# Kernel optimization log

Hardware: AMD Instinct MI355X
Metric: run time of the kernel (lower is better)

The kernel has to match this reference:

```python
import jax, jax.numpy as jnp
import numpy as np

H = 100
N = 262144

def setup_inputs() -> dict:
    key = jax.random.key(0)
    ks = jax.random.split(key, 9)
    s = 1.0 / np.sqrt(H)
    return {
        "m": jax.random.normal(ks[0], (1, H), jnp.float32),
        "output_hidden": jax.random.normal(ks[1], (1, 1, H), jnp.float32),
        "fact_embeddings": jax.random.normal(ks[2], (N, H), jnp.float32),
        "W1": jax.random.normal(ks[3], (H, 2 * H), jnp.float32) * s,
        "b1": jax.random.normal(ks[4], (H,), jnp.float32) * s,
        "W2": jax.random.normal(ks[5], (1, H), jnp.float32) * s,
        "b2": jax.random.normal(ks[6], (1,), jnp.float32) * s,
        "W3": jax.random.normal(ks[7], (H, 3 * H), jnp.float32) * s,
        "b3": jax.random.normal(ks[8], (H,), jnp.float32) * s,
    }

def reference(m, output_hidden, fact_embeddings, W1, b1, W2, b2, W3, b3):
    output_context = output_hidden[0]                      # [1, H]
    # z = [|f - oh| ; |f - m|]  -> [N, 2H] (broadcast over N)
    z = jnp.concatenate(
        [jnp.abs(fact_embeddings - output_context),
         jnp.abs(fact_embeddings - m)], axis=1)
    # MLP attention scores, softmax over N facts
    g = jnp.tanh(z @ W1.T + b1) @ W2.T + b2                # [N, 1]
    g = jax.nn.softmax(g.ravel())                          # [N]
    # Weighted-sum pooling of facts
    c = (g[:, None] * fact_embeddings).sum(axis=0, keepdims=True)  # [1, H]
    # Gated memory update
    m_new = jax.nn.relu(jnp.concatenate([m, c, output_context], axis=1) @ W3.T + b3)
    return m_new
```

## Files before the change

kernel.cpp:

```cpp
#include <hip/hip_runtime.h>
#include <hip/hip_bf16.h>
#include <math.h>

#define HDIM 100
#define NFACT 262144
#define FPB   128
#define NBLK_T 2048
#define TPB   4
#define GRID  (NBLK_T / TPB)
#define NTHREADS 512

#define KHALF 112
#define NJT 7
#define NKC 7
#define NBFRAG (NJT * NKC * 64)

#define NCOPY 116
#define NSTRIPE 4

using short8 = __attribute__((ext_vector_type(8))) short;
using f32x4  = __attribute__((ext_vector_type(4))) float;

#define WS_B    0
#define WS_ACC  12544

__device__ __forceinline__ unsigned short f2bf(float x) {
    unsigned u = __builtin_bit_cast(unsigned, x);
    u += 0x7FFFu + ((u >> 16) & 1u);
    return (unsigned short)(u >> 16);
}

__device__ __forceinline__ float tanh_fast(float x) {
    float e = __expf(2.0f * x);
    return 1.0f - 2.0f / (1.0f + e);
}

__global__ __launch_bounds__(256) void k_prep_b(const float* __restrict__ W1,
                                                float* __restrict__ ws) {
    int tg = blockIdx.x * 256 + threadIdx.x;
    if (tg < NSTRIPE * NCOPY) ws[WS_ACC + tg] = 0.f;
    if (tg >= NBFRAG) return;
    int lane = tg & 63;
    int kc = (tg >> 6) % NKC;
    int jt = tg / (NKC * 64);
    int g = lane >> 4, r = lane & 15;
    int j = jt * 16 + r;
    unsigned short v[8];
    #pragma unroll
    for (int e = 0; e < 8; e++) {
        int kglob = kc * 32 + g * 8 + e;
        int half = (kglob >= KHALF) ? 1 : 0;
        int koff = kglob - half * KHALF;
        float x = 0.f;
        if (j < HDIM && koff < HDIM) x = W1[j * 200 + half * HDIM + koff];
        v[e] = f2bf(x);
    }
    uint4 d;
    d.x = (unsigned)v[0] | ((unsigned)v[1] << 16);
    d.y = (unsigned)v[2] | ((unsigned)v[3] << 16);
    d.z = (unsigned)v[4] | ((unsigned)v[5] << 16);
    d.w = (unsigned)v[6] | ((unsigned)v[7] << 16);
    ((uint4*)(ws + WS_B))[tg] = d;
}

__device__ __forceinline__ float4 ld4c(const float* p, bool ok) {
    float4 z = make_float4(0.f, 0.f, 0.f, 0.f);
    return ok ? *(const float4*)p : z;
}

__device__ __forceinline__ uint4 pack_diff_u(float4 a0, float4 a1,
                                             float4 b0, float4 b1) {
    union { __hip_bfloat16 h[8]; uint4 u; } u;
    u.h[0] = __float2bfloat16(a0.x - b0.x); u.h[1] = __float2bfloat16(a0.y - b0.y);
    u.h[2] = __float2bfloat16(a0.z - b0.z); u.h[3] = __float2bfloat16(a0.w - b0.w);
    u.h[4] = __float2bfloat16(a1.x - b1.x); u.h[5] = __float2bfloat16(a1.y - b1.y);
    u.h[6] = __float2bfloat16(a1.z - b1.z); u.h[7] = __float2bfloat16(a1.w - b1.w);
    return u.u;
}

__device__ __forceinline__ uint4 and_mask(uint4 u) {
    u.x &= 0x7FFF7FFFu; u.y &= 0x7FFF7FFFu;
    u.z &= 0x7FFF7FFFu; u.w &= 0x7FFF7FFFu;
    return u;
}

__device__ __forceinline__ float4 shfl32_f4(float4 v) {
    float4 r;
    r.x = __shfl_xor(v.x, 32); r.y = __shfl_xor(v.y, 32);
    r.z = __shfl_xor(v.z, 32); r.w = __shfl_xor(v.w, 32);
    return r;
}

template<int CTRL>
__device__ __forceinline__ float dpp_radd(float x) {
    int y = __builtin_amdgcn_update_dpp(0, __builtin_bit_cast(int, x),
                                        CTRL, 0xF, 0xF, true);
    return x + __builtin_bit_cast(float, y);
}
__device__ __forceinline__ float row_reduce16(float x) {
    x = dpp_radd<0x121>(x);
    x = dpp_radd<0x122>(x);
    x = dpp_radd<0x124>(x);
    x = dpp_radd<0x128>(x);
    return x;
}

__global__ __launch_bounds__(NTHREADS, 2) void k_logits(
        const float* __restrict__ fe,
        const float* __restrict__ oc,
        const float* __restrict__ mvec,
        const float* __restrict__ b1,
        const float* __restrict__ W2,
        float* __restrict__ ws) {
    __shared__ __align__(16) uint4 Bs[NBFRAG];
    __shared__ float poolS[KHALF];
    __shared__ float cpad[2 * KHALF];
    __shared__ float bw[2 * KHALF];
    __shared__ float sS;

    int t = threadIdx.x;
    int w = t >> 6, lane = t & 63, g = lane >> 4, r = lane & 15;
    bool ghi = (lane & 32) != 0;

    if (t == 0) sS = 0.f;
    if (t < KHALF) poolS[t] = 0.f;

    if (t < 2 * KHALF) {
        int half = t / KHALF, k = t % KHALF;
        cpad[t] = (k < HDIM) ? (half ? mvec[k] : oc[k]) : 0.f;
        bw[t]   = (k < HDIM) ? (half ? W2[k]   : b1[k]) : 0.f;
    }

    {
        const uint4* Bg = (const uint4*)(ws + WS_B);
        #pragma unroll
        for (int i = 0; i < 7; i++) {
            int base = i * 512 + w * 64;
            if (base < NBFRAG) {
                __builtin_amdgcn_global_load_lds(
                    (const __attribute__((address_space(1))) unsigned int*)(Bg + base + lane),
                    (__attribute__((address_space(3))) unsigned int*)(Bs + base),
                    16, 0, 0);
            }
        }
    }
    __syncthreads();

    float sacc = 0.f;
    float p[4][8];
    #pragma unroll
    for (int c = 0; c < 4; c++)
        #pragma unroll
        for (int e = 0; e < 8; e++) p[c][e] = 0.f;

    #pragma unroll 1
    for (int tt = 0; tt < TPB; tt++) {
        int tile = blockIdx.x * TPB + tt;
        long n0 = (long)tile * FPB;
        const float* fp = fe + (n0 + w * 16 + r) * HDIM;

        float4 f0c[4], f1c[4];
        if (tile != NBLK_T - 1) {
            #pragma unroll
            for (int kc = 0; kc < 4; kc++) {
                int col = kc * 32 + g * 8;
                f0c[kc] = *(const float4*)(fp + col);
                f1c[kc] = *(const float4*)(fp + col + 4);
            }
        } else {
            #pragma unroll
            for (int kc = 0; kc < 4; kc++) {
                int col = kc * 32 + g * 8;
                f0c[kc] = ld4c(fp + col, col < HDIM);
                f1c[kc] = ld4c(fp + col + 4, col + 4 < HDIM);
            }
        }

        uint4 zsig[4];
        #pragma unroll
        for (int kc = 0; kc < 4; kc++) {
            int pk = kc * 32 + g * 8;
            float4 s0 = *(const float4*)(cpad + pk);
            float4 s1 = *(const float4*)(cpad + pk + 4);
            zsig[kc] = pack_diff_u(f0c[kc], f1c[kc], s0, s1);
        }

        uint4 zabsHi[3];
        #pragma unroll
        for (int c = 0; c < 3; c++) {
            int pk = (4 + c) * 32 + g * 8;
            float4 sa0 = ghi ? f0c[c] : f0c[c + 1];
            float4 sa1 = ghi ? f1c[c] : f1c[c + 1];
            float4 ra0 = shfl32_f4(sa0);
            float4 ra1 = shfl32_f4(sa1);
            float4 s0 = *(const float4*)(cpad + pk);
            float4 s1 = *(const float4*)(cpad + pk + 4);
            zabsHi[c] = and_mask(pack_diff_u(ra0, ra1, s0, s1));
        }

        float gacc = 0.f;
        #pragma unroll
        for (int jt = 0; jt < NJT; jt++) {
            int jb = jt * 16 + g * 4;
            float4 b1q = *(const float4*)(bw + jb);
            float4 w2q = *(const float4*)(bw + KHALF + jb);
            f32x4 acc = {b1q.x, b1q.y, b1q.z, b1q.w};
            #pragma unroll
            for (int kc = 0; kc < NKC; kc++) {
                short8 av = __builtin_bit_cast(short8, Bs[(jt * NKC + kc) * 64 + lane]);
                uint4 bu = (kc < 4) ? and_mask(zsig[kc]) : zabsHi[kc - 4];
                acc = __builtin_amdgcn_mfma_f32_16x16x32_bf16(
                    av, __builtin_bit_cast(short8, bu), acc, 0, 0, 0);
            }
            gacc = fmaf(tanh_fast(acc[0]), w2q.x, gacc);
            gacc = fmaf(tanh_fast(acc[1]), w2q.y, gacc);
            gacc = fmaf(tanh_fast(acc[2]), w2q.z, gacc);
            gacc = fmaf(tanh_fast(acc[3]), w2q.w, gacc);
        }
        gacc += __shfl_xor(gacc, 16);
        gacc += __shfl_xor(gacc, 32);
        float w_r = __expf(gacc);

        sacc += w_r;

        #pragma unroll
        for (int c = 0; c < 4; c++) {
            union { uint4 u; unsigned short us[8]; } uz; uz.u = zsig[c];
            #pragma unroll
            for (int e = 0; e < 8; e++) {
                float zf = __builtin_bit_cast(float, ((unsigned)uz.us[e]) << 16);
                p[c][e] = fmaf(w_r, zf, p[c][e]);
            }
        }

        __builtin_amdgcn_sched_barrier(0);
    }

    #pragma unroll
    for (int c = 0; c < 4; c++)
        #pragma unroll
        for (int e = 0; e < 8; e++) p[c][e] = row_reduce16(p[c][e]);
    float s16 = row_reduce16(sacc);
    if (lane == 0) atomicAdd(&sS, s16);

    if (r == 0) {
        #pragma unroll
        for (int c = 0; c < 4; c++) {
            int pk = c * 32 + g * 8;
            if (pk < KHALF) {
                #pragma unroll
                for (int e = 0; e < 8; e++)
                    atomicAdd(&poolS[pk + e], p[c][e]);
            }
        }
    }
    __syncthreads();

    int cp = (blockIdx.x & (NSTRIPE - 1)) * NCOPY;
    if (t < KHALF && t < HDIM) atomicAdd(&ws[WS_ACC + cp + t], poolS[t]);
    if (t == 0) atomicAdd(&ws[WS_ACC + cp + KHALF], sS);
}

__global__ __launch_bounds__(128) void k_final(
        const float* __restrict__ mvec,
        const float* __restrict__ oc,
        const float* __restrict__ W3,
        const float* __restrict__ b3,
        const float* __restrict__ ws,
        float* __restrict__ out) {
    __shared__ float vv[300];
    int t = threadIdx.x;
    float S = 0.f;
    #pragma unroll
    for (int i = 0; i < NSTRIPE; i++) S += ws[WS_ACC + i * NCOPY + KHALF];
    if (t < HDIM) {
        float corr = 0.f;
        #pragma unroll
        for (int i = 0; i < NSTRIPE; i++) corr += ws[WS_ACC + i * NCOPY + t];
        vv[t] = mvec[t];
        vv[HDIM + t] = oc[t] + corr / S;
        vv[2 * HDIM + t] = oc[t];
    }
    __syncthreads();
    if (t < HDIM) {
        float a = b3[t];
        const float* wr = W3 + t * 3 * HDIM;
        #pragma unroll 4
        for (int k = 0; k < 3 * HDIM; k++) a = fmaf(wr[k], vv[k], a);
        out[t] = fmaxf(a, 0.f);
    }
}

extern "C" void kernel_launch(void* const* d_in, const int* in_sizes, int n_in,
                              void* d_out, int out_size, void* d_ws, size_t ws_size,
                              hipStream_t stream) {
    const float* mvec = (const float*)d_in[0];
    const float* oh   = (const float*)d_in[1];
    const float* fe   = (const float*)d_in[2];
    const float* W1   = (const float*)d_in[3];
    const float* b1   = (const float*)d_in[4];
    const float* W2   = (const float*)d_in[5];
    const float* W3   = (const float*)d_in[7];
    const float* b3   = (const float*)d_in[8];
    float* ws  = (float*)d_ws;
    float* out = (float*)d_out;

    k_prep_b<<<13, 256, 0, stream>>>(W1, ws);
    k_logits<<<GRID, NTHREADS, 0, stream>>>(fe, oh, mvec, b1, W2, ws);
    k_final<<<1, 128, 0, stream>>>(mvec, oh, W3, b3, ws, out);
}
```

Measured before the change: 78.70 us.

## Double-buffer fact tile loads in registers and reduce pooling per tile

```diff
diff --git a/kernel.cpp b/kernel.cpp
--- a/kernel.cpp
+++ b/kernel.cpp
@@ -144,38 +144,33 @@
             }
         }
     }
-    __syncthreads();
+
+    int row_off = w * 16 + r;
+
+    auto issue_load = [&](int tile, float4* f0, float4* f1) {
+        const float* fp = fe + ((long)tile * FPB + row_off) * HDIM;
+        if (tile != NBLK_T - 1) {
+            #pragma unroll
+            for (int kc = 0; kc < 4; kc++) {
+                int pk = kc * 32 + g * 8;
+                int col = (pk >= KHALF) ? (pk - KHALF) : pk;
+                f0[kc] = *(const float4*)(fp + col);
+                f1[kc] = *(const float4*)(fp + col + 4);
+            }
+        } else {
+            #pragma unroll
+            for (int kc = 0; kc < 4; kc++) {
+                int pk = kc * 32 + g * 8;
+                int col = (pk >= KHALF) ? (pk - KHALF) : pk;
+                f0[kc] = ld4c(fp + col, col < HDIM);
+                f1[kc] = ld4c(fp + col + 4, col + 4 < HDIM);
+            }
+        }
+    };
 
     float sacc = 0.f;
-    float p[4][8];
-    #pragma unroll
-    for (int c = 0; c < 4; c++)
-        #pragma unroll
-        for (int e = 0; e < 8; e++) p[c][e] = 0.f;
-
-    #pragma unroll 1
-    for (int tt = 0; tt < TPB; tt++) {
-        int tile = blockIdx.x * TPB + tt;
-        long n0 = (long)tile * FPB;
-        const float* fp = fe + (n0 + w * 16 + r) * HDIM;
-
-        float4 f0c[4], f1c[4];
-        if (tile != NBLK_T - 1) {
-            #pragma unroll
-            for (int kc = 0; kc < 4; kc++) {
-                int col = kc * 32 + g * 8;
-                f0c[kc] = *(const float4*)(fp + col);
-                f1c[kc] = *(const float4*)(fp + col + 4);
-            }
-        } else {
-            #pragma unroll
-            for (int kc = 0; kc < 4; kc++) {
-                int col = kc * 32 + g * 8;
-                f0c[kc] = ld4c(fp + col, col < HDIM);
-                f1c[kc] = ld4c(fp + col + 4, col + 4 < HDIM);
-            }
-        }
-
+
+    auto process = [&](float4* f0c, float4* f1c) {
         uint4 zsig[4];
         #pragma unroll
         for (int kc = 0; kc < 4; kc++) {
@@ -184,7 +179,6 @@
             float4 s1 = *(const float4*)(cpad + pk + 4);
             zsig[kc] = pack_diff_u(f0c[kc], f1c[kc], s0, s1);
         }
-
         uint4 zabsHi[3];
         #pragma unroll
         for (int c = 0; c < 3; c++) {
@@ -220,40 +214,57 @@
         gacc += __shfl_xor(gacc, 16);
         gacc += __shfl_xor(gacc, 32);
         float w_r = __expf(gacc);
-
         sacc += w_r;
 
+        float p[4][8];
         #pragma unroll
         for (int c = 0; c < 4; c++) {
             union { uint4 u; unsigned short us[8]; } uz; uz.u = zsig[c];
             #pragma unroll
             for (int e = 0; e < 8; e++) {
                 float zf = __builtin_bit_cast(float, ((unsigned)uz.us[e]) << 16);
-                p[c][e] = fmaf(w_r, zf, p[c][e]);
-            }
-        }
-
-        __builtin_amdgcn_sched_barrier(0);
-    }
-
-    #pragma unroll
-    for (int c = 0; c < 4; c++)
-        #pragma unroll
-        for (int e = 0; e < 8; e++) p[c][e] = row_reduce16(p[c][e]);
+                p[c][e] = w_r * zf;
+            }
+        }
+        #pragma unroll
+        for (int c = 0; c < 4; c++)
+            #pragma unroll
+            for (int e = 0; e < 8; e++) p[c][e] = row_reduce16(p[c][e]);
+        if (r == 0) {
+            #pragma unroll
+            for (int c = 0; c < 4; c++) {
+                int pk = c * 32 + g * 8;
+                if (pk < KHALF) {
+                    #pragma unroll
+                    for (int e = 0; e < 8; e++)
+                        atomicAdd(&poolS[pk + e], p[c][e]);
+                }
+            }
+        }
+    };
+
+    int tile0 = blockIdx.x * TPB;
+    float4 fA0[4], fA1[4], fB0[4], fB1[4];
+
+    issue_load(tile0 + 0, fA0, fA1);
+    __syncthreads();
+
+    issue_load(tile0 + 1, fB0, fB1);
+    process(fA0, fA1);
+    __builtin_amdgcn_sched_barrier(0);
+
+    issue_load(tile0 + 2, fA0, fA1);
+    process(fB0, fB1);
+    __builtin_amdgcn_sched_barrier(0);
+
+    issue_load(tile0 + 3, fB0, fB1);
+    process(fA0, fA1);
+    __builtin_amdgcn_sched_barrier(0);
+
+    process(fB0, fB1);
+
     float s16 = row_reduce16(sacc);
     if (lane == 0) atomicAdd(&sS, s16);
-
-    if (r == 0) {
-        #pragma unroll
-        for (int c = 0; c < 4; c++) {
-            int pk = c * 32 + g * 8;
-            if (pk < KHALF) {
-                #pragma unroll
-                for (int e = 0; e < 8; e++)
-                    atomicAdd(&poolS[pk + e], p[c][e]);
-            }
-        }
-    }
     __syncthreads();
 
     int cp = (blockIdx.x & (NSTRIPE - 1)) * NCOPY;
```

Result: faster. 75.62 us (-3.9%).
